# Kernel optimization log

Measured on AMD Instinct MI355X. Metric: run time of the kernel, lower is better.

## Reference

```python
import jax, jax.numpy as jnp
import numpy as np

N = 50000
E = 800000
IN_FEATS = 256
OUT_FEATS = 128
NEG_SLOPE = 0.2
ALPHA = 0.5


def segment_softmax(x, seg, num_segments):
    # numerically-stable softmax over edges grouped by destination node
    m = jax.ops.segment_max(x, seg, num_segments=num_segments)
    z = jnp.exp(x - m[seg])
    s = jax.ops.segment_sum(z, seg, num_segments=num_segments)
    return z / s[seg]


def setup_inputs() -> dict:
    key = jax.random.key(0)
    ks = jax.random.split(key, 8)
    feat = jax.random.normal(ks[0], (N, IN_FEATS), dtype=jnp.float32)
    w = jax.random.normal(ks[1], (E,), dtype=jnp.float32)
    fc_w = jax.random.normal(ks[2], (IN_FEATS, OUT_FEATS), dtype=jnp.float32) * (1.0 / np.sqrt(IN_FEATS))
    attn_l = jax.random.normal(ks[3], (1, 1, OUT_FEATS), dtype=jnp.float32) * 0.1
    attn_r = jax.random.normal(ks[4], (1, 1, OUT_FEATS), dtype=jnp.float32) * 0.1
    bias_param = jnp.zeros((OUT_FEATS,), dtype=jnp.float32)
    src = jax.random.randint(ks[5], (E,), 0, N, dtype=jnp.int32)
    dst = jax.random.randint(ks[6], (E,), 0, N, dtype=jnp.int32)
    return {"feat": feat, "w": w, "fc_w": fc_w, "attn_l": attn_l,
            "attn_r": attn_r, "bias_param": bias_param, "src": src, "dst": dst}


def reference(feat, w, fc_w, attn_l, attn_r, bias_param, src, dst):
    # fc projection: [N, H=1, D]
    ft = (feat @ fc_w).reshape(N, 1, OUT_FEATS)
    # per-node attention logits [N, 1]
    el = (ft * attn_l).sum(-1)
    er = (ft * attn_r).sum(-1)
    # u_add_v edge scores + leaky relu: [E, 1]
    e = el[src] + er[dst]
    e = jnp.where(e > 0, e, NEG_SLOPE * e)
    # edge_softmax over destination neighborhoods (per head); H==1 so squeeze to [E]
    a = segment_softmax(e[:, 0], dst, N)
    # edge_softmax of precomputed edge weight 'w'
    ws = segment_softmax(w, dst, N)
    # blend attentions
    a = a * (1.0 - ALPHA) + ws * ALPHA
    # u_mul_e + sum aggregation: [E,1,D] messages -> [N,1,D]
    m = ft[src] * a[:, None, None]
    rst = jax.ops.segment_sum(m, dst, num_segments=N)
    rst = rst + bias_param.reshape(1, 1, OUT_FEATS)
    return rst
```

## Files before the change

### kernel.cpp

```cpp
#include <hip/hip_runtime.h>

#define NN 50000
#define NE 800000
#define KIN 256
#define DOUT 128
#define NEG_SLOPE 0.2f
#define ALPHA 0.5f
#define ELL_CAP 48

typedef __attribute__((ext_vector_type(8))) short bf16x8;
typedef __attribute__((ext_vector_type(4))) float f32x4;

__device__ __forceinline__ unsigned short f2b(float v) {
  unsigned int u = __float_as_uint(v);
  return (unsigned short)((u + 0x7fffu + ((u >> 16) & 1u)) >> 16);
}
__device__ __forceinline__ float b2f(unsigned short h) {
  return __uint_as_float(((unsigned int)h) << 16);
}
__device__ __forceinline__ unsigned short f2h(float v) {
  _Float16 h = (_Float16)v;
  return __builtin_bit_cast(unsigned short, h);
}
__device__ __forceinline__ float h2f(unsigned short u) {
  return (float)__builtin_bit_cast(_Float16, u);
}

__global__ void prep_b(const float* __restrict__ fc_w, unsigned short* __restrict__ b_hi,
                       unsigned short* __restrict__ b_lo) {
  int t = blockIdx.x * 256 + threadIdx.x;
  if (t >= KIN * DOUT) return;
  int k = t >> 7, c = t & 127;
  float v = fc_w[t];
  unsigned short h = f2b(v);
  unsigned short l = f2b(v - b2f(h));
  int kt = k >> 5, kl = k & 31;
  int g = kl >> 3, j = kl & 7;
  int idx = ((kt * 128 + c) * 4 + g) * 8 + j;
  b_hi[idx] = h;
  b_lo[idx] = l;
}

__global__ __launch_bounds__(256) void gemm_ft(
    const float* __restrict__ feat, const unsigned short* __restrict__ b_hi,
    const unsigned short* __restrict__ b_lo, const float* __restrict__ attn_l,
    const float* __restrict__ attn_r, unsigned short* __restrict__ ft16,
    float* __restrict__ el, float* __restrict__ er) {
  const int tid = threadIdx.x;
  const int lane = tid & 63;
  const int wv = tid >> 6;
  const int cl = lane & 15;
  const int g = lane >> 4;
  const int row = blockIdx.x * 64 + wv * 16 + cl;
  const size_t arow = (size_t)min(row, NN - 1) * KIN;
  const int boff0 = cl * 32 + g * 8;

  f32x4 acc[8];
#pragma unroll
  for (int ct = 0; ct < 8; ++ct) acc[ct] = (f32x4){0.f, 0.f, 0.f, 0.f};

#pragma unroll
  for (int kt = 0; kt < 8; ++kt) {
    const float* ap = feat + arow + kt * 32 + g * 8;
    float4 a0 = *(const float4*)ap;
    float4 a1 = *(const float4*)(ap + 4);
    bf16x8 ah, alo;
    {
      float f[8] = {a0.x, a0.y, a0.z, a0.w, a1.x, a1.y, a1.z, a1.w};
#pragma unroll
      for (int j = 0; j < 8; ++j) {
        unsigned short h = f2b(f[j]);
        ah[j] = (short)h;
        alo[j] = (short)f2b(f[j] - b2f(h));
      }
    }
    const unsigned short* bh = b_hi + kt * 4096 + boff0;
    const unsigned short* bl = b_lo + kt * 4096 + boff0;
#pragma unroll
    for (int ct = 0; ct < 8; ++ct) {
      bf16x8 bhv = *(const bf16x8*)(bh + ct * 512);
      bf16x8 blv = *(const bf16x8*)(bl + ct * 512);
      acc[ct] = __builtin_amdgcn_mfma_f32_16x16x32_bf16(ah, bhv, acc[ct], 0, 0, 0);
      acc[ct] = __builtin_amdgcn_mfma_f32_16x16x32_bf16(alo, bhv, acc[ct], 0, 0, 0);
      acc[ct] = __builtin_amdgcn_mfma_f32_16x16x32_bf16(ah, blv, acc[ct], 0, 0, 0);
    }
  }

  float pl[4] = {0, 0, 0, 0}, pr[4] = {0, 0, 0, 0};
  const int r0 = blockIdx.x * 64 + wv * 16 + g * 4;
#pragma unroll
  for (int ct = 0; ct < 8; ++ct) {
    int col = ct * 16 + cl;
    float av = attn_l[col];
    float bv = attn_r[col];
#pragma unroll
    for (int q = 0; q < 4; ++q) {
      float v = acc[ct][q];
      int r = r0 + q;
      if (r < NN) ft16[(size_t)r * DOUT + col] = f2b(v);
      pl[q] = fmaf(v, av, pl[q]);
      pr[q] = fmaf(v, bv, pr[q]);
    }
  }
#pragma unroll
  for (int q = 0; q < 4; ++q) {
    float a = pl[q], b = pr[q];
#pragma unroll
    for (int d = 1; d < 16; d <<= 1) {
      a += __shfl_xor(a, d);
      b += __shfl_xor(b, d);
    }
    if (cl == 0) {
      int r = r0 + q;
      if (r < NN) { el[r] = a; er[r] = b; }
    }
  }
}

__global__ void edge_ell(const int* __restrict__ src, const int* __restrict__ dst,
                         const float* __restrict__ w, int* __restrict__ deg,
                         unsigned int* __restrict__ ell) {
  int t = blockIdx.x * 256 + threadIdx.x;
  int e0 = t * 4;
  if (e0 >= NE) return;
  int4 s4 = *(const int4*)(src + e0);
  int4 d4 = *(const int4*)(dst + e0);
  float4 w4 = *(const float4*)(w + e0);
  int p0 = atomicAdd(&deg[d4.x], 1);
  int p1 = atomicAdd(&deg[d4.y], 1);
  int p2 = atomicAdd(&deg[d4.z], 1);
  int p3 = atomicAdd(&deg[d4.w], 1);
  if (p0 < ELL_CAP) ell[d4.x * ELL_CAP + p0] = ((unsigned)s4.x << 16) | f2h(w4.x);
  if (p1 < ELL_CAP) ell[d4.y * ELL_CAP + p1] = ((unsigned)s4.y << 16) | f2h(w4.y);
  if (p2 < ELL_CAP) ell[d4.z * ELL_CAP + p2] = ((unsigned)s4.z << 16) | f2h(w4.z);
  if (p3 < ELL_CAP) ell[d4.w * ELL_CAP + p3] = ((unsigned)s4.w << 16) | f2h(w4.w);
}

__global__ __launch_bounds__(256) void aggregate(
    const unsigned short* __restrict__ ft16, const unsigned int* __restrict__ ell,
    const int* __restrict__ deg, const float* __restrict__ el,
    const float* __restrict__ er, const float* __restrict__ bias,
    float* __restrict__ out) {
  const int lane = threadIdx.x & 63;
  const int wv = threadIdx.x >> 6;
  const int n = blockIdx.x * 4 + wv;
  if (n >= NN) return;
  const int dg = min(deg[n], ELL_CAP);
  const float ern = er[n];

  float z = 0.f, zw = 0.f;
  int so = 0;
  if (lane < dg) {
    unsigned int ent = ell[n * ELL_CAP + lane];
    int s = (int)(ent >> 16);
    so = s * DOUT;
    float x = el[s] + ern;
    x = (x > 0.f) ? x : NEG_SLOPE * x;
    z = __expf(x);
    zw = __expf(h2f((unsigned short)(ent & 0xffffu)));
  }
  float se = z, sw = zw;
#pragma unroll
  for (int d = 1; d < 64; d <<= 1) {
    se += __shfl_xor(se, d);
    sw += __shfl_xor(sw, d);
  }
  const float coef = z * ((1.f - ALPHA) / se) + zw * (ALPHA / sw);

  float acc[8] = {0.f, 0.f, 0.f, 0.f, 0.f, 0.f, 0.f, 0.f};
  const unsigned short* ftp = ft16 + (lane & 15) * 8;
  for (int jb = 0; jb < dg; jb += 4) {
    int j = jb + (lane >> 4);
    float cj = __shfl(coef, j);
    int soj = __shfl(so, j);
    bf16x8 row = *(const bf16x8*)(ftp + soj);
#pragma unroll
    for (int c = 0; c < 8; ++c)
      acc[c] = fmaf(cj, b2f((unsigned short)row[c]), acc[c]);
  }
#pragma unroll
  for (int c = 0; c < 8; ++c) {
    acc[c] += __shfl_xor(acc[c], 16);
    acc[c] += __shfl_xor(acc[c], 32);
  }
  if (lane < 16) {
    const float4 b0 = *(const float4*)(bias + lane * 8);
    const float4 b1 = *(const float4*)(bias + lane * 8 + 4);
    float4 o0, o1;
    o0.x = acc[0] + b0.x; o0.y = acc[1] + b0.y; o0.z = acc[2] + b0.z; o0.w = acc[3] + b0.w;
    o1.x = acc[4] + b1.x; o1.y = acc[5] + b1.y; o1.z = acc[6] + b1.z; o1.w = acc[7] + b1.w;
    float* op = out + (size_t)n * DOUT + lane * 8;
    *(float4*)op = o0;
    *(float4*)(op + 4) = o1;
  }
}

extern "C" void kernel_launch(void* const* d_in, const int* in_sizes, int n_in,
                              void* d_out, int out_size, void* d_ws, size_t ws_size,
                              hipStream_t stream) {
  const float* feat = (const float*)d_in[0];
  const float* w = (const float*)d_in[1];
  const float* fc_w = (const float*)d_in[2];
  const float* attn_l = (const float*)d_in[3];
  const float* attn_r = (const float*)d_in[4];
  const float* bias = (const float*)d_in[5];
  const int* src = (const int*)d_in[6];
  const int* dst = (const int*)d_in[7];
  float* out = (float*)d_out;

  char* ws = (char*)d_ws;
  size_t o = 0;
  auto take = [&](size_t bytes) {
    char* p = ws + o;
    o = (o + bytes + 255) & ~(size_t)255;
    return p;
  };
  unsigned short* ft16 = (unsigned short*)take((size_t)NN * DOUT * 2);
  float* el = (float*)take((size_t)NN * 4);
  float* er = (float*)take((size_t)NN * 4);
  unsigned short* b_hi = (unsigned short*)take((size_t)KIN * DOUT * 2);
  unsigned short* b_lo = (unsigned short*)take((size_t)KIN * DOUT * 2);
  int* deg = (int*)take((size_t)NN * 4);
  unsigned int* ell = (unsigned int*)take((size_t)NN * ELL_CAP * 4);

  hipMemsetAsync(deg, 0, (size_t)NN * 4, stream);
  prep_b<<<(KIN * DOUT + 255) / 256, 256, 0, stream>>>(fc_w, b_hi, b_lo);
  edge_ell<<<(NE / 4 + 255) / 256, 256, 0, stream>>>(src, dst, w, deg, ell);
  gemm_ft<<<(NN + 63) / 64, 256, 0, stream>>>(feat, b_hi, b_lo, attn_l, attn_r, ft16, el, er);
  aggregate<<<(NN + 3) / 4, 256, 0, stream>>>(ft16, ell, deg, el, er, bias, out);
}
```

Measured before the change: 223.9 us.

## Replace atomic ELL build with two-level bucketed counting sort by destination group

Replaces the global-atomic ELL construction with a per-block histogram over 64-node destination groups, a multi-kernel prefix scan, and a scatter into a compact edge buffer using shared-memory atomics. The aggregation kernel then loads each group's edges into LDS, sorts them locally by node, and runs the same softmax and gather per node. The aim is to remove contended global atomics and the scattered writes to a padded ELL array. In exchange it adds several kernel launches and a second pass over the edges, and it silently drops edges when a group exceeds 1536 or a node exceeds 64.

Result: no change. 220.8 us (-1.4%).

```diff
diff --git a/kernel.cpp b/kernel.cpp
--- a/kernel.cpp
+++ b/kernel.cpp
@@ -6,7 +6,14 @@
 #define DOUT 128
 #define NEG_SLOPE 0.2f
 #define ALPHA 0.5f
-#define ELL_CAP 48
+
+#define GB 6
+#define GSZ 64
+#define NG ((NN + GSZ - 1) / GSZ)
+#define EPB 8192
+#define NB ((NE + EPB - 1) / EPB)
+#define HTOT (NG * NB)
+#define GCAP 1536
 
 typedef __attribute__((ext_vector_type(8))) short bf16x8;
 typedef __attribute__((ext_vector_type(4))) float f32x4;
@@ -117,81 +124,196 @@
   }
 }
 
-__global__ void edge_ell(const int* __restrict__ src, const int* __restrict__ dst,
-                         const float* __restrict__ w, int* __restrict__ deg,
-                         unsigned int* __restrict__ ell) {
-  int t = blockIdx.x * 256 + threadIdx.x;
-  int e0 = t * 4;
-  if (e0 >= NE) return;
-  int4 s4 = *(const int4*)(src + e0);
-  int4 d4 = *(const int4*)(dst + e0);
-  float4 w4 = *(const float4*)(w + e0);
-  int p0 = atomicAdd(&deg[d4.x], 1);
-  int p1 = atomicAdd(&deg[d4.y], 1);
-  int p2 = atomicAdd(&deg[d4.z], 1);
-  int p3 = atomicAdd(&deg[d4.w], 1);
-  if (p0 < ELL_CAP) ell[d4.x * ELL_CAP + p0] = ((unsigned)s4.x << 16) | f2h(w4.x);
-  if (p1 < ELL_CAP) ell[d4.y * ELL_CAP + p1] = ((unsigned)s4.y << 16) | f2h(w4.y);
-  if (p2 < ELL_CAP) ell[d4.z * ELL_CAP + p2] = ((unsigned)s4.z << 16) | f2h(w4.z);
-  if (p3 < ELL_CAP) ell[d4.w * ELL_CAP + p3] = ((unsigned)s4.w << 16) | f2h(w4.w);
-}
-
-__global__ __launch_bounds__(256) void aggregate(
-    const unsigned short* __restrict__ ft16, const unsigned int* __restrict__ ell,
-    const int* __restrict__ deg, const float* __restrict__ el,
+__global__ __launch_bounds__(256) void k_hist(const int* __restrict__ dst,
+                                              int* __restrict__ hist) {
+  __shared__ int lh[NG];
+  const int tid = threadIdx.x, b = blockIdx.x;
+  for (int i = tid; i < NG; i += 256) lh[i] = 0;
+  __syncthreads();
+  const int base = b * EPB;
+#pragma unroll
+  for (int it = 0; it < EPB / 1024; ++it) {
+    int e = base + it * 1024 + tid * 4;
+    if (e < NE) {
+      int4 d4 = *(const int4*)(dst + e);
+      atomicAdd(&lh[d4.x >> GB], 1);
+      atomicAdd(&lh[d4.y >> GB], 1);
+      atomicAdd(&lh[d4.z >> GB], 1);
+      atomicAdd(&lh[d4.w >> GB], 1);
+    }
+  }
+  __syncthreads();
+  for (int i = tid; i < NG; i += 256) hist[i * NB + b] = lh[i];
+}
+
+__global__ void scan_blk(const int* __restrict__ in, int* __restrict__ out,
+                         int* __restrict__ bsums, int n) {
+  __shared__ int s[256];
+  int tid = threadIdx.x;
+  int base = blockIdx.x * 2048 + tid * 8;
+  int v[8];
+  int tot = 0;
+#pragma unroll
+  for (int j = 0; j < 8; ++j) {
+    int i = base + j;
+    v[j] = (i < n) ? in[i] : 0;
+    tot += v[j];
+  }
+  s[tid] = tot;
+  __syncthreads();
+  for (int d = 1; d < 256; d <<= 1) {
+    int t = (tid >= d) ? s[tid - d] : 0;
+    __syncthreads();
+    s[tid] += t;
+    __syncthreads();
+  }
+  int run = s[tid] - tot;
+  if (tid == 255) bsums[blockIdx.x] = s[255];
+#pragma unroll
+  for (int j = 0; j < 8; ++j) {
+    int i = base + j;
+    if (i < n) out[i] = run;
+    run += v[j];
+  }
+}
+
+__global__ void scan_tops(int* __restrict__ bsums, int nb) {
+  int l = threadIdx.x;
+  int v = (l < nb) ? bsums[l] : 0;
+  int inc = v;
+#pragma unroll
+  for (int d = 1; d < 64; d <<= 1) {
+    int t = __shfl_up(inc, d);
+    if (l >= d) inc += t;
+  }
+  if (l < nb) bsums[l] = inc - v;
+}
+
+__global__ void scan_add2(int* __restrict__ out, const int* __restrict__ bsums, int n) {
+  int i = blockIdx.x * 256 + threadIdx.x;
+  if (i < n) out[i] += bsums[i >> 11];
+}
+
+__global__ __launch_bounds__(256) void k_scatter(
+    const int* __restrict__ src, const int* __restrict__ dst, const float* __restrict__ w,
+    const int* __restrict__ S, uint2* __restrict__ ebuf) {
+  __shared__ int cur[NG];
+  const int tid = threadIdx.x, b = blockIdx.x;
+  for (int i = tid; i < NG; i += 256) cur[i] = S[i * NB + b];
+  __syncthreads();
+  const int base = b * EPB;
+#pragma unroll
+  for (int it = 0; it < EPB / 1024; ++it) {
+    int e = base + it * 1024 + tid * 4;
+    if (e < NE) {
+      int4 s4 = *(const int4*)(src + e);
+      int4 d4 = *(const int4*)(dst + e);
+      float4 w4 = *(const float4*)(w + e);
+      int p0 = atomicAdd(&cur[d4.x >> GB], 1);
+      ebuf[p0] = make_uint2(((unsigned)s4.x << 16) | f2h(w4.x), (unsigned)d4.x);
+      int p1 = atomicAdd(&cur[d4.y >> GB], 1);
+      ebuf[p1] = make_uint2(((unsigned)s4.y << 16) | f2h(w4.y), (unsigned)d4.y);
+      int p2 = atomicAdd(&cur[d4.z >> GB], 1);
+      ebuf[p2] = make_uint2(((unsigned)s4.z << 16) | f2h(w4.z), (unsigned)d4.z);
+      int p3 = atomicAdd(&cur[d4.w >> GB], 1);
+      ebuf[p3] = make_uint2(((unsigned)s4.w << 16) | f2h(w4.w), (unsigned)d4.w);
+    }
+  }
+}
+
+__global__ __launch_bounds__(256) void agg(
+    const unsigned short* __restrict__ ft16, const uint2* __restrict__ ebuf,
+    const int* __restrict__ S, const float* __restrict__ el,
     const float* __restrict__ er, const float* __restrict__ bias,
     float* __restrict__ out) {
-  const int lane = threadIdx.x & 63;
-  const int wv = threadIdx.x >> 6;
-  const int n = blockIdx.x * 4 + wv;
-  if (n >= NN) return;
-  const int dg = min(deg[n], ELL_CAP);
-  const float ern = er[n];
-
-  float z = 0.f, zw = 0.f;
-  int so = 0;
-  if (lane < dg) {
-    unsigned int ent = ell[n * ELL_CAP + lane];
-    int s = (int)(ent >> 16);
-    so = s * DOUT;
-    float x = el[s] + ern;
-    x = (x > 0.f) ? x : NEG_SLOPE * x;
-    z = __expf(x);
-    zw = __expf(h2f((unsigned short)(ent & 0xffffu)));
-  }
-  float se = z, sw = zw;
-#pragma unroll
-  for (int d = 1; d < 64; d <<= 1) {
-    se += __shfl_xor(se, d);
-    sw += __shfl_xor(sw, d);
-  }
-  const float coef = z * ((1.f - ALPHA) / se) + zw * (ALPHA / sw);
-
-  float acc[8] = {0.f, 0.f, 0.f, 0.f, 0.f, 0.f, 0.f, 0.f};
-  const unsigned short* ftp = ft16 + (lane & 15) * 8;
-  for (int jb = 0; jb < dg; jb += 4) {
-    int j = jb + (lane >> 4);
-    float cj = __shfl(coef, j);
-    int soj = __shfl(so, j);
-    bf16x8 row = *(const bf16x8*)(ftp + soj);
-#pragma unroll
-    for (int c = 0; c < 8; ++c)
-      acc[c] = fmaf(cj, b2f((unsigned short)row[c]), acc[c]);
-  }
-#pragma unroll
-  for (int c = 0; c < 8; ++c) {
-    acc[c] += __shfl_xor(acc[c], 16);
-    acc[c] += __shfl_xor(acc[c], 32);
-  }
-  if (lane < 16) {
-    const float4 b0 = *(const float4*)(bias + lane * 8);
-    const float4 b1 = *(const float4*)(bias + lane * 8 + 4);
-    float4 o0, o1;
-    o0.x = acc[0] + b0.x; o0.y = acc[1] + b0.y; o0.z = acc[2] + b0.z; o0.w = acc[3] + b0.w;
-    o1.x = acc[4] + b1.x; o1.y = acc[5] + b1.y; o1.z = acc[6] + b1.z; o1.w = acc[7] + b1.w;
-    float* op = out + (size_t)n * DOUT + lane * 8;
-    *(float4*)op = o0;
-    *(float4*)(op + 4) = o1;
+  __shared__ uint2 ents[GCAP];
+  __shared__ unsigned int sorted[GCAP];
+  __shared__ int lh[GSZ], pfx[GSZ], cu[GSZ];
+  const int g = blockIdx.x, tid = threadIdx.x;
+  const int gbeg = S[g * NB];
+  const int gend = (g == NG - 1) ? NE : S[(g + 1) * NB];
+  const int cnt = min(gend - gbeg, GCAP);
+
+  if (tid < GSZ) lh[tid] = 0;
+  __syncthreads();
+  for (int i = tid; i < cnt; i += 256) {
+    uint2 en = ebuf[gbeg + i];
+    ents[i] = en;
+    atomicAdd(&lh[en.y & (GSZ - 1)], 1);
+  }
+  __syncthreads();
+  if (tid < GSZ) {
+    int v = lh[tid];
+    int inc = v;
+#pragma unroll
+    for (int d = 1; d < 64; d <<= 1) {
+      int t = __shfl_up(inc, d);
+      if (tid >= d) inc += t;
+    }
+    pfx[tid] = inc - v;
+    cu[tid] = inc - v;
+  }
+  __syncthreads();
+  for (int i = tid; i < cnt; i += 256) {
+    uint2 en = ents[i];
+    int pos = atomicAdd(&cu[en.y & (GSZ - 1)], 1);
+    sorted[pos] = en.x;
+  }
+  __syncthreads();
+
+  const int lane = tid & 63;
+  const int wv = tid >> 6;
+  for (int ld = wv; ld < GSZ; ld += 4) {
+    int node = g * GSZ + ld;
+    if (node >= NN) continue;
+    int beg = pfx[ld];
+    int dg = min(lh[ld], 64);
+    float ern = er[node];
+    float z = 0.f, zw = 0.f;
+    int so = 0;
+    if (lane < dg) {
+      unsigned u = sorted[beg + lane];
+      int s = (int)(u >> 16);
+      so = s * DOUT;
+      float x = el[s] + ern;
+      x = (x > 0.f) ? x : NEG_SLOPE * x;
+      z = __expf(x);
+      zw = __expf(h2f((unsigned short)(u & 0xffffu)));
+    }
+    float se = z, sw = zw;
+#pragma unroll
+    for (int d = 1; d < 64; d <<= 1) {
+      se += __shfl_xor(se, d);
+      sw += __shfl_xor(sw, d);
+    }
+    float coef = z * ((1.f - ALPHA) / se) + zw * (ALPHA / sw);
+
+    float acc[8] = {0.f, 0.f, 0.f, 0.f, 0.f, 0.f, 0.f, 0.f};
+    const unsigned short* ftp = ft16 + (lane & 15) * 8;
+    for (int jb = 0; jb < dg; jb += 4) {
+      int j = jb + (lane >> 4);
+      float cj = __shfl(coef, j);
+      int soj = __shfl(so, j);
+      bf16x8 row = *(const bf16x8*)(ftp + soj);
+#pragma unroll
+      for (int c = 0; c < 8; ++c)
+        acc[c] = fmaf(cj, b2f((unsigned short)row[c]), acc[c]);
+    }
+#pragma unroll
+    for (int c = 0; c < 8; ++c) {
+      acc[c] += __shfl_xor(acc[c], 16);
+      acc[c] += __shfl_xor(acc[c], 32);
+    }
+    if (lane < 16) {
+      const float4 b0 = *(const float4*)(bias + lane * 8);
+      const float4 b1 = *(const float4*)(bias + lane * 8 + 4);
+      float4 o0, o1;
+      o0.x = acc[0] + b0.x; o0.y = acc[1] + b0.y; o0.z = acc[2] + b0.z; o0.w = acc[3] + b0.w;
+      o1.x = acc[4] + b1.x; o1.y = acc[5] + b1.y; o1.z = acc[6] + b1.z; o1.w = acc[7] + b1.w;
+      float* op = out + (size_t)node * DOUT + lane * 8;
+      *(float4*)op = o0;
+      *(float4*)(op + 4) = o1;
+    }
   }
 }
 
@@ -220,12 +342,18 @@
   float* er = (float*)take((size_t)NN * 4);
   unsigned short* b_hi = (unsigned short*)take((size_t)KIN * DOUT * 2);
   unsigned short* b_lo = (unsigned short*)take((size_t)KIN * DOUT * 2);
-  int* deg = (int*)take((size_t)NN * 4);
-  unsigned int* ell = (unsigned int*)take((size_t)NN * ELL_CAP * 4);
-
-  hipMemsetAsync(deg, 0, (size_t)NN * 4, stream);
+  int* hist = (int*)take((size_t)HTOT * 4);
+  int* S = (int*)take((size_t)HTOT * 4);
+  int* bsums = (int*)take(256);
+  uint2* ebuf = (uint2*)take((size_t)NE * 8);
+
+  const int nsb = (HTOT + 2047) / 2048;
   prep_b<<<(KIN * DOUT + 255) / 256, 256, 0, stream>>>(fc_w, b_hi, b_lo);
-  edge_ell<<<(NE / 4 + 255) / 256, 256, 0, stream>>>(src, dst, w, deg, ell);
+  k_hist<<<NB, 256, 0, stream>>>(dst, hist);
+  scan_blk<<<nsb, 256, 0, stream>>>(hist, S, bsums, HTOT);
+  scan_tops<<<1, 64, 0, stream>>>(bsums, nsb);
+  scan_add2<<<(HTOT + 255) / 256, 256, 0, stream>>>(S, bsums, HTOT);
+  k_scatter<<<NB, 256, 0, stream>>>(src, dst, w, S, ebuf);
   gemm_ft<<<(NN + 63) / 64, 256, 0, stream>>>(feat, b_hi, b_lo, attn_l, attn_r, ft16, el, er);
-  aggregate<<<(NN + 3) / 4, 256, 0, stream>>>(ft16, ell, deg, el, er, bias, out);
-}
+  agg<<<NG, 256, 0, stream>>>(ft16, ebuf, S, el, er, bias, out);
+}
```

## Fuse edge ELL build into GEMM kernel and unroll aggregation gathers

Applied to the files above, without the earlier changes.

Merges the edge-to-ELL scatter kernel and the projection GEMM into one launch. Blocks are interleaved four edge blocks to one GEMM block, so the atomic-heavy scatter can overlap with the MFMA work and one launch is saved. The aggregation loop now issues four independent row gathers per iteration instead of one, putting more memory loads in flight. In exchange, each edge thread handles a single edge with scalar loads instead of vectorized int4 loads, and the unrolled loop pads with zero-coefficient rows up to a multiple of 16 neighbours.

New measurement: 207.0 us. 7.5% less time.

```diff
diff --git a/kernel.cpp b/kernel.cpp
--- a/kernel.cpp
+++ b/kernel.cpp
@@ -7,6 +7,9 @@
 #define NEG_SLOPE 0.2f
 #define ALPHA 0.5f
 #define ELL_CAP 48
+
+#define GEMM_BLKS ((NN + 63) / 64)
+#define FUSED_BLKS (GEMM_BLKS * 5)
 
 typedef __attribute__((ext_vector_type(8))) short bf16x8;
 typedef __attribute__((ext_vector_type(4))) float f32x4;
@@ -41,17 +44,33 @@
   b_lo[idx] = l;
 }
 
-__global__ __launch_bounds__(256) void gemm_ft(
+__global__ __launch_bounds__(256) void fused_front(
     const float* __restrict__ feat, const unsigned short* __restrict__ b_hi,
     const unsigned short* __restrict__ b_lo, const float* __restrict__ attn_l,
     const float* __restrict__ attn_r, unsigned short* __restrict__ ft16,
-    float* __restrict__ el, float* __restrict__ er) {
+    float* __restrict__ el, float* __restrict__ er,
+    const int* __restrict__ src, const int* __restrict__ dst,
+    const float* __restrict__ w, int* __restrict__ deg,
+    unsigned int* __restrict__ ell) {
+  const int r = blockIdx.x % 5;
+  const int q = blockIdx.x / 5;
+
+  if (r != 4) {
+    int e = (q * 4 + r) * 256 + threadIdx.x;
+    if (e < NE) {
+      int d = dst[e];
+      int p = atomicAdd(&deg[d], 1);
+      if (p < ELL_CAP) ell[d * ELL_CAP + p] = ((unsigned)src[e] << 16) | f2h(w[e]);
+    }
+    return;
+  }
+
   const int tid = threadIdx.x;
   const int lane = tid & 63;
   const int wv = tid >> 6;
   const int cl = lane & 15;
   const int g = lane >> 4;
-  const int row = blockIdx.x * 64 + wv * 16 + cl;
+  const int row = q * 64 + wv * 16 + cl;
   const size_t arow = (size_t)min(row, NN - 1) * KIN;
   const int boff0 = cl * 32 + g * 8;
 
@@ -87,56 +106,37 @@
   }
 
   float pl[4] = {0, 0, 0, 0}, pr[4] = {0, 0, 0, 0};
-  const int r0 = blockIdx.x * 64 + wv * 16 + g * 4;
+  const int r0 = q * 64 + wv * 16 + g * 4;
 #pragma unroll
   for (int ct = 0; ct < 8; ++ct) {
     int col = ct * 16 + cl;
     float av = attn_l[col];
     float bv = attn_r[col];
 #pragma unroll
-    for (int q = 0; q < 4; ++q) {
-      float v = acc[ct][q];
-      int r = r0 + q;
-      if (r < NN) ft16[(size_t)r * DOUT + col] = f2b(v);
-      pl[q] = fmaf(v, av, pl[q]);
-      pr[q] = fmaf(v, bv, pr[q]);
-    }
-  }
-#pragma unroll
-  for (int q = 0; q < 4; ++q) {
-    float a = pl[q], b = pr[q];
+    for (int qq = 0; qq < 4; ++qq) {
+      float v = acc[ct][qq];
+      int rr = r0 + qq;
+      if (rr < NN) ft16[(size_t)rr * DOUT + col] = f2b(v);
+      pl[qq] = fmaf(v, av, pl[qq]);
+      pr[qq] = fmaf(v, bv, pr[qq]);
+    }
+  }
+#pragma unroll
+  for (int qq = 0; qq < 4; ++qq) {
+    float a = pl[qq], b = pr[qq];
 #pragma unroll
     for (int d = 1; d < 16; d <<= 1) {
       a += __shfl_xor(a, d);
       b += __shfl_xor(b, d);
     }
     if (cl == 0) {
-      int r = r0 + q;
-      if (r < NN) { el[r] = a; er[r] = b; }
-    }
-  }
-}
-
-__global__ void edge_ell(const int* __restrict__ src, const int* __restrict__ dst,
-                         const float* __restrict__ w, int* __restrict__ deg,
-                         unsigned int* __restrict__ ell) {
-  int t = blockIdx.x * 256 + threadIdx.x;
-  int e0 = t * 4;
-  if (e0 >= NE) return;
-  int4 s4 = *(const int4*)(src + e0);
-  int4 d4 = *(const int4*)(dst + e0);
-  float4 w4 = *(const float4*)(w + e0);
-  int p0 = atomicAdd(&deg[d4.x], 1);
-  int p1 = atomicAdd(&deg[d4.y], 1);
-  int p2 = atomicAdd(&deg[d4.z], 1);
-  int p3 = atomicAdd(&deg[d4.w], 1);
-  if (p0 < ELL_CAP) ell[d4.x * ELL_CAP + p0] = ((unsigned)s4.x << 16) | f2h(w4.x);
-  if (p1 < ELL_CAP) ell[d4.y * ELL_CAP + p1] = ((unsigned)s4.y << 16) | f2h(w4.y);
-  if (p2 < ELL_CAP) ell[d4.z * ELL_CAP + p2] = ((unsigned)s4.z << 16) | f2h(w4.z);
-  if (p3 < ELL_CAP) ell[d4.w * ELL_CAP + p3] = ((unsigned)s4.w << 16) | f2h(w4.w);
-}
-
-__global__ __launch_bounds__(256) void aggregate(
+      int rr = r0 + qq;
+      if (rr < NN) { el[rr] = a; er[rr] = b; }
+    }
+  }
+}
+
+__global__ __launch_bounds__(256) void agg(
     const unsigned short* __restrict__ ft16, const unsigned int* __restrict__ ell,
     const int* __restrict__ deg, const float* __restrict__ el,
     const float* __restrict__ er, const float* __restrict__ bias,
@@ -151,13 +151,13 @@
   float z = 0.f, zw = 0.f;
   int so = 0;
   if (lane < dg) {
-    unsigned int ent = ell[n * ELL_CAP + lane];
-    int s = (int)(ent >> 16);
+    unsigned u = ell[n * ELL_CAP + lane];
+    int s = (int)(u >> 16);
     so = s * DOUT;
     float x = el[s] + ern;
     x = (x > 0.f) ? x : NEG_SLOPE * x;
     z = __expf(x);
-    zw = __expf(h2f((unsigned short)(ent & 0xffffu)));
+    zw = __expf(h2f((unsigned short)(u & 0xffffu)));
   }
   float se = z, sw = zw;
 #pragma unroll
@@ -169,14 +169,24 @@
 
   float acc[8] = {0.f, 0.f, 0.f, 0.f, 0.f, 0.f, 0.f, 0.f};
   const unsigned short* ftp = ft16 + (lane & 15) * 8;
-  for (int jb = 0; jb < dg; jb += 4) {
-    int j = jb + (lane >> 4);
-    float cj = __shfl(coef, j);
-    int soj = __shfl(so, j);
-    bf16x8 row = *(const bf16x8*)(ftp + soj);
-#pragma unroll
-    for (int c = 0; c < 8; ++c)
-      acc[c] = fmaf(cj, b2f((unsigned short)row[c]), acc[c]);
+  const int lg = lane >> 4;
+  for (int jb = 0; jb < dg; jb += 16) {
+    int j0 = jb + lg;
+    float c0 = __shfl(coef, j0), c1 = __shfl(coef, j0 + 4);
+    float c2 = __shfl(coef, j0 + 8), c3 = __shfl(coef, j0 + 12);
+    int s0 = __shfl(so, j0), s1 = __shfl(so, j0 + 4);
+    int s2 = __shfl(so, j0 + 8), s3 = __shfl(so, j0 + 12);
+    bf16x8 r0 = *(const bf16x8*)(ftp + s0);
+    bf16x8 r1 = *(const bf16x8*)(ftp + s1);
+    bf16x8 r2 = *(const bf16x8*)(ftp + s2);
+    bf16x8 r3 = *(const bf16x8*)(ftp + s3);
+#pragma unroll
+    for (int c = 0; c < 8; ++c) {
+      acc[c] = fmaf(c0, b2f((unsigned short)r0[c]), acc[c]);
+      acc[c] = fmaf(c1, b2f((unsigned short)r1[c]), acc[c]);
+      acc[c] = fmaf(c2, b2f((unsigned short)r2[c]), acc[c]);
+      acc[c] = fmaf(c3, b2f((unsigned short)r3[c]), acc[c]);
+    }
   }
 #pragma unroll
   for (int c = 0; c < 8; ++c) {
@@ -225,7 +235,7 @@
 
   hipMemsetAsync(deg, 0, (size_t)NN * 4, stream);
   prep_b<<<(KIN * DOUT + 255) / 256, 256, 0, stream>>>(fc_w, b_hi, b_lo);
-  edge_ell<<<(NE / 4 + 255) / 256, 256, 0, stream>>>(src, dst, w, deg, ell);
-  gemm_ft<<<(NN + 63) / 64, 256, 0, stream>>>(feat, b_hi, b_lo, attn_l, attn_r, ft16, el, er);
-  aggregate<<<(NN + 3) / 4, 256, 0, stream>>>(ft16, ell, deg, el, er, bias, out);
-}
+  fused_front<<<FUSED_BLKS, 256, 0, stream>>>(feat, b_hi, b_lo, attn_l, attn_r, ft16,
+                                              el, er, src, dst, w, deg, ell);
+  agg<<<(NN + 3) / 4, 256, 0, stream>>>(ft16, ell, deg, el, er, bias, out);
+}
```
